# Performance work log

Measured on AMD Instinct MI355X. Metric: run time of the kernel, lower is better.

The kernel has to match this reference:

```python
import jax, jax.numpy as jnp
import numpy as np

B, T, C, H = 4, 4096, 1024, 64

def setup_inputs() -> dict:
    key = jax.random.key(0)
    k1, k2, k3, k4, k5 = jax.random.split(key, 5)
    scale = 0.02
    return {
        "x": jax.random.normal(k1, (B, T, C), dtype=jnp.float32),
        "head_bias": jax.random.normal(k2, (T, T), dtype=jnp.float32) * 0.1,
        "w_k": jax.random.normal(k3, (C, H), dtype=jnp.float32) * scale,
        "w_q": jax.random.normal(k4, (C, H), dtype=jnp.float32) * scale,
        "w_v": jax.random.normal(k5, (C, H), dtype=jnp.float32) * scale,
    }

def reference(x, head_bias, w_k, w_q, w_v):
    # x: (B,T,C) ; projections: (B,T,H)
    k = jnp.einsum('btc,ch->bth', x, w_k)
    q = jnp.einsum('btc,ch->bth', x, w_q)
    v = jnp.einsum('btc,ch->bth', x, w_v)
    Tq = x.shape[1]
    # scores: (B,T,T) with RPE bias and causal mask
    scores = jnp.einsum('bqh,bkh->bqk', q, k) * (k.shape[-1] ** -0.5)
    scores = scores + head_bias[None, :, :]
    causal = jnp.tril(jnp.ones((Tq, Tq), dtype=bool))
    scores = jnp.where(causal[None, :, :], scores, -jnp.inf)
    weights = jax.nn.softmax(scores, axis=-1)
    out = jnp.einsum('bqk,bkh->bqh', weights, v)
    return out
```

## Files before the change

kernel.cpp:

```cpp
#include <hip/hip_runtime.h>
#include <hip/hip_bf16.h>


#define T_DIM 4096
#define C_DIM 1024
#define QT    64
#define KT    64
#define CK    512

typedef __attribute__((ext_vector_type(8))) short s16x8;
typedef __attribute__((ext_vector_type(4))) float f32x4;
typedef __attribute__((ext_vector_type(2))) unsigned int u32x2;

__device__ __forceinline__ short f2bf(float f) {
    unsigned u = __builtin_bit_cast(unsigned, f);
    u += 0x7FFFu + ((u >> 16) & 1u);
    return (short)(u >> 16);
}
__device__ __forceinline__ unsigned pack2(float a, float b) {
    unsigned ua = __builtin_bit_cast(unsigned, a);
    unsigned ub = __builtin_bit_cast(unsigned, b);
    ua += 0x7FFFu + ((ua >> 16) & 1u);
    ub += 0x7FFFu + ((ub >> 16) & 1u);
    return __builtin_amdgcn_perm(ub, ua, 0x07060302u);
}
__device__ __forceinline__ float bf2f(short s) {
    unsigned u = ((unsigned)(unsigned short)s) << 16;
    return __builtin_bit_cast(float, u);
}

__global__ __launch_bounds__(256) void prep_frag(
    const float* __restrict__ wk, const float* __restrict__ wq,
    const float* __restrict__ wv, short* __restrict__ wfrag)
{
    int ksAll = blockIdx.x, mat = blockIdx.y;
    const float* w = (mat == 0) ? wk : ((mat == 1) ? wq : wv);
    float sc = (mat == 1) ? 0.125f : 1.0f;
    int nt = threadIdx.x >> 6, lane = threadIdx.x & 63;
    int quad = lane >> 4, l15 = lane & 15;
    int h = nt * 16 + l15;
    int cb = ksAll * 32 + quad * 8;
    s16x8 v;
    #pragma unroll
    for (int j = 0; j < 8; ++j) v[j] = f2bf(w[(cb + j) * 64 + h] * sc);
    *(s16x8*)&wfrag[((ksAll * 12 + mat * 4 + nt) * 64 + lane) * 8] = v;
}

__global__ __launch_bounds__(256, 2) void proj_part(
    const float* __restrict__ x, const short* __restrict__ wfrag,
    short* __restrict__ pp)
{
    int w = threadIdx.x >> 6, lane = threadIdx.x & 63;
    int l15 = lane & 15, quad = lane >> 4;
    int row0 = (blockIdx.x * 4 + w) * 16;
    int cq = blockIdx.y;

    f32x4 acc[12];
    #pragma unroll
    for (int i = 0; i < 12; ++i) acc[i] = (f32x4){0.f, 0.f, 0.f, 0.f};

    const float* xrow = x + (size_t)(row0 + l15) * C_DIM + cq * 256;

    #pragma unroll
    for (int ks = 0; ks < 8; ++ks) {
        int ksAll = cq * 8 + ks;
        const s16x8* fb = (const s16x8*)&wfrag[(size_t)(ksAll * 12 * 64 + lane) * 8];
        f32x4 x0 = *(const f32x4*)(xrow + ks * 32 + quad * 8);
        f32x4 x1 = *(const f32x4*)(xrow + ks * 32 + quad * 8 + 4);
        s16x8 af;
        unsigned p0 = pack2(x0[0], x0[1]), p1 = pack2(x0[2], x0[3]);
        unsigned p2 = pack2(x1[0], x1[1]), p3 = pack2(x1[2], x1[3]);
        af[0] = (short)p0; af[1] = (short)(p0 >> 16);
        af[2] = (short)p1; af[3] = (short)(p1 >> 16);
        af[4] = (short)p2; af[5] = (short)(p2 >> 16);
        af[6] = (short)p3; af[7] = (short)(p3 >> 16);
        #pragma unroll
        for (int f = 0; f < 12; ++f) {
            s16x8 bf = fb[f * 64];
            acc[f] = __builtin_amdgcn_mfma_f32_16x16x32_bf16(af, bf, acc[f], 0, 0, 0);
        }
    }
    short* base = pp + (size_t)cq * 16384 * 192;
    #pragma unroll
    for (int f = 0; f < 12; ++f) {
        int mat = f >> 2, nt = f & 3;
        #pragma unroll
        for (int r = 0; r < 4; ++r)
            base[(size_t)(row0 + quad * 4 + r) * 192 + mat * 64 + nt * 16 + l15] =
                f2bf(acc[f][r]);
    }
}

__global__ __launch_bounds__(256) void proj_combine(
    const short* __restrict__ pp, short* __restrict__ kb,
    short* __restrict__ qb, short* __restrict__ vtb)
{
    int m0 = blockIdx.x * 64;
    __shared__ short vt[64][72];
    #pragma unroll
    for (int o = 0; o < 6; ++o) {
        int oct = o * 256 + threadIdx.x;
        int row = oct / 24, c8 = (oct - row * 24) * 8;
        float s[8];
        #pragma unroll
        for (int j = 0; j < 8; ++j) s[j] = 0.f;
        #pragma unroll
        for (int cq = 0; cq < 4; ++cq) {
            s16x8 v = *(const s16x8*)&pp[((size_t)cq * 16384 + m0 + row) * 192 + c8];
            #pragma unroll
            for (int j = 0; j < 8; ++j) s[j] += bf2f(v[j]);
        }
        s16x8 r;
        #pragma unroll
        for (int j = 0; j < 4; ++j) {
            unsigned d = pack2(s[2 * j], s[2 * j + 1]);
            r[2 * j] = (short)d; r[2 * j + 1] = (short)(d >> 16);
        }
        if (c8 < 64)        *(s16x8*)&kb[(size_t)(m0 + row) * 64 + c8] = r;
        else if (c8 < 128)  *(s16x8*)&qb[(size_t)(m0 + row) * 64 + (c8 - 64)] = r;
        else {
            #pragma unroll
            for (int j = 0; j < 8; ++j) vt[c8 - 128 + j][row] = r[j];
        }
    }
    __syncthreads();
    int b = m0 >> 12, t0 = m0 & 4095;
    #pragma unroll
    for (int o = 0; o < 2; ++o) {
        int oct = o * 256 + threadIdx.x;
        int h = oct >> 3, tl = (oct & 7) * 8;
        s16x8 v = *(const s16x8*)&vt[h][tl];
        *(s16x8*)&vtb[(((size_t)b * 64 + h) << 12) + t0 + tl] = v;
    }
}

__global__ __launch_bounds__(256) void flash_part(
    const short* __restrict__ qb, const short* __restrict__ kb,
    const short* __restrict__ vtb, const float* __restrict__ bias,
    short* __restrict__ po)
{
    int qt = blockIdx.x, c = blockIdx.y, b = blockIdx.z;
    int q0 = qt * QT;
    int kstart = c * CK;
    int kend = min(kstart + CK, q0 + QT);
    if (kstart >= kend) return;

    __shared__ __align__(16) short klds[64][72];
    __shared__ __align__(16) short vlds[64][72];
    __shared__ __align__(16) short plds[4][16][72];

    int w = threadIdx.x >> 6, lane = threadIdx.x & 63;
    int l15 = lane & 15, quad = lane >> 4;
    int strip0 = q0 + w * 16;

    const short* qrow = qb + (size_t)(b * T_DIM + strip0 + l15) * 64;
    s16x8 aq0 = *(const s16x8*)(qrow + quad * 8);
    s16x8 aq1 = *(const s16x8*)(qrow + 32 + quad * 8);

    float l_sum = 0.f;
    f32x4 accO[4];
    #pragma unroll
    for (int nt = 0; nt < 4; ++nt) accO[nt] = (f32x4){0.f, 0.f, 0.f, 0.f};

    const float* brow = bias + (size_t)(strip0 + l15) * T_DIM;

    for (int k0 = kstart; k0 < kend; k0 += KT) {
        f32x4 vb[4];
        #pragma unroll
        for (int nt = 0; nt < 4; ++nt)
            vb[nt] = *(const f32x4*)&brow[k0 + nt * 16 + quad * 4];

        __syncthreads();
        #pragma unroll
        for (int rep = 0; rep < 4; ++rep) {
            int cid = threadIdx.x + rep * 256;
            int rem = cid & 511, row = rem >> 3, ch = rem & 7;
            if (cid < 512)
                *(s16x8*)&klds[row][ch * 8] =
                    *(const s16x8*)&kb[(size_t)(b * T_DIM + k0 + row) * 64 + ch * 8];
            else
                *(s16x8*)&vlds[row][ch * 8] =
                    *(const s16x8*)&vtb[(((size_t)b * 64 + row) << 12) + k0 + ch * 8];
        }
        __syncthreads();

        f32x4 accS[4];
        #pragma unroll
        for (int nt = 0; nt < 4; ++nt) accS[nt] = (f32x4){0.f, 0.f, 0.f, 0.f};
        #pragma unroll
        for (int nt = 0; nt < 4; ++nt) {
            s16x8 a0 = *(const s16x8*)&klds[nt * 16 + l15][quad * 8];
            accS[nt] = __builtin_amdgcn_mfma_f32_16x16x32_bf16(a0, aq0, accS[nt], 0, 0, 0);
            s16x8 a1 = *(const s16x8*)&klds[nt * 16 + l15][32 + quad * 8];
            accS[nt] = __builtin_amdgcn_mfma_f32_16x16x32_bf16(a1, aq1, accS[nt], 0, 0, 0);
        }

        int qrow_g = strip0 + l15;
        bool diag = (k0 + KT - 1 > strip0);
        #pragma unroll
        for (int nt = 0; nt < 4; ++nt) {
            float sv[4];
            #pragma unroll
            for (int r = 0; r < 4; ++r) {
                sv[r] = accS[nt][r] + vb[nt][r];
                if (diag && (k0 + nt * 16 + quad * 4 + r > qrow_g))
                    sv[r] = -__builtin_inff();
                float p = __expf(sv[r]);
                sv[r] = p;
                l_sum += p;
            }
            u32x2 d;
            d[0] = pack2(sv[0], sv[1]);
            d[1] = pack2(sv[2], sv[3]);
            *(u32x2*)&plds[w][l15][nt * 16 + quad * 4] = d;
        }

        s16x8 ap0 = *(const s16x8*)&plds[w][l15][quad * 8];
        s16x8 ap1 = *(const s16x8*)&plds[w][l15][32 + quad * 8];
        #pragma unroll
        for (int nt = 0; nt < 4; ++nt) {
            s16x8 bv0 = *(const s16x8*)&vlds[nt * 16 + l15][quad * 8];
            accO[nt] = __builtin_amdgcn_mfma_f32_16x16x32_bf16(ap0, bv0, accO[nt], 0, 0, 0);
            s16x8 bv1 = *(const s16x8*)&vlds[nt * 16 + l15][32 + quad * 8];
            accO[nt] = __builtin_amdgcn_mfma_f32_16x16x32_bf16(ap1, bv1, accO[nt], 0, 0, 0);
        }
    }

    l_sum += __shfl_xor(l_sum, 16, 64);
    l_sum += __shfl_xor(l_sum, 32, 64);

    short* base = po + (size_t)(((b * 64 + qt) * 8) + c) * 4160;
    #pragma unroll
    for (int nt = 0; nt < 4; ++nt)
        #pragma unroll
        for (int r = 0; r < 4; ++r)
            base[(w * 16 + quad * 4 + r) * 64 + nt * 16 + l15] = f2bf(accO[nt][r]);
    if (quad == 0) base[4096 + w * 16 + l15] = f2bf(l_sum);
}

__global__ __launch_bounds__(256) void flash_reduce(
    const short* __restrict__ po, float* __restrict__ out)
{
    int idx = blockIdx.x * 256 + threadIdx.x;
    int row = idx >> 4, c4 = idx & 15;
    int b = row >> 12, t = row & 4095;
    int qt = t >> 6, rloc = t & 63;
    int nc = (t >> 9) + 1;
    float o0 = 0.f, o1 = 0.f, o2 = 0.f, o3 = 0.f, l = 0.f;
    for (int cc = 0; cc < nc; ++cc) {
        const short* base = po + (size_t)(((b * 64 + qt) * 8) + cc) * 4160;
        const short* p = &base[rloc * 64 + c4 * 4];
        o0 += bf2f(p[0]); o1 += bf2f(p[1]); o2 += bf2f(p[2]); o3 += bf2f(p[3]);
        l += bf2f(base[4096 + rloc]);
    }
    float inv = 1.0f / l;
    f32x4 res = (f32x4){o0 * inv, o1 * inv, o2 * inv, o3 * inv};
    *(f32x4*)&out[(size_t)row * 64 + c4 * 4] = res;
}

extern "C" void kernel_launch(void* const* d_in, const int* in_sizes, int n_in,
                              void* d_out, int out_size, void* d_ws, size_t ws_size,
                              hipStream_t stream) {
    (void)in_sizes; (void)n_in; (void)out_size; (void)ws_size;
    const float* x    = (const float*)d_in[0];
    const float* bias = (const float*)d_in[1];
    const float* wk   = (const float*)d_in[2];
    const float* wq   = (const float*)d_in[3];
    const float* wv   = (const float*)d_in[4];
    float* out = (float*)d_out;

    short* wfrag = (short*)d_ws;
    short* kb    = wfrag + 196608;
    short* qb    = kb + 1048576;
    short* vtb   = qb + 1048576;
    short* pp    = vtb + 1048576;
    short* po    = pp + (size_t)12582912;

    prep_frag<<<dim3(32, 3), dim3(256), 0, stream>>>(wk, wq, wv, wfrag);
    proj_part<<<dim3(256, 4), dim3(256), 0, stream>>>(x, wfrag, pp);
    proj_combine<<<dim3(256), dim3(256), 0, stream>>>(pp, kb, qb, vtb);
    flash_part<<<dim3(64, 8, 4), dim3(256), 0, stream>>>(qb, kb, vtb, bias, po);
    flash_reduce<<<dim3(1024), dim3(256), 0, stream>>>(po, out);
}
```

Measured before the change: 221.8 us.

## Load K/V MFMA fragments directly from global memory, drop LDS staging

The flash kernel no longer stages K and V^T tiles through shared memory with two block barriers per tile. Each wave now loads its MFMA operand fragments straight from global memory, so the four waves fetch the same K/V data redundantly and rely on L1/L2 caching. The projection kernel drops its occupancy hint, stops unrolling the C-chunk loop, and rotates the starting chunk per block to spread weight-fragment reads. The trade is fewer barriers and less LDS traffic against more global/cache loads and higher register pressure.

```diff
diff --git a/kernel.cpp b/kernel.cpp
--- a/kernel.cpp
+++ b/kernel.cpp
@@ -46,7 +46,7 @@
     *(s16x8*)&wfrag[((ksAll * 12 + mat * 4 + nt) * 64 + lane) * 8] = v;
 }
 
-__global__ __launch_bounds__(256, 2) void proj_part(
+__global__ __launch_bounds__(256) void proj_part(
     const float* __restrict__ x, const short* __restrict__ wfrag,
     short* __restrict__ pp)
 {
@@ -61,8 +61,9 @@
 
     const float* xrow = x + (size_t)(row0 + l15) * C_DIM + cq * 256;
 
-    #pragma unroll
-    for (int ks = 0; ks < 8; ++ks) {
+    #pragma unroll 1
+    for (int ksi = 0; ksi < 8; ++ksi) {
+        int ks = (ksi + blockIdx.x) & 7;
         int ksAll = cq * 8 + ks;
         const s16x8* fb = (const s16x8*)&wfrag[(size_t)(ksAll * 12 * 64 + lane) * 8];
         f32x4 x0 = *(const f32x4*)(xrow + ks * 32 + quad * 8);
@@ -145,8 +146,6 @@
     int kend = min(kstart + CK, q0 + QT);
     if (kstart >= kend) return;
 
-    __shared__ __align__(16) short klds[64][72];
-    __shared__ __align__(16) short vlds[64][72];
     __shared__ __align__(16) short plds[4][16][72];
 
     int w = threadIdx.x >> 6, lane = threadIdx.x & 63;
@@ -163,36 +162,36 @@
     for (int nt = 0; nt < 4; ++nt) accO[nt] = (f32x4){0.f, 0.f, 0.f, 0.f};
 
     const float* brow = bias + (size_t)(strip0 + l15) * T_DIM;
-
+    const short* kbb  = kb + ((size_t)b * T_DIM) * 64;
+    const short* vbb  = vtb + ((size_t)b * 64 << 12);
+
+    #pragma unroll 1
     for (int k0 = kstart; k0 < kend; k0 += KT) {
+        s16x8 ak0[4], ak1[4];
+        #pragma unroll
+        for (int nt = 0; nt < 4; ++nt) {
+            const short* kr = kbb + (size_t)(k0 + nt * 16 + l15) * 64;
+            ak0[nt] = *(const s16x8*)(kr + quad * 8);
+            ak1[nt] = *(const s16x8*)(kr + 32 + quad * 8);
+        }
         f32x4 vb[4];
         #pragma unroll
         for (int nt = 0; nt < 4; ++nt)
             vb[nt] = *(const f32x4*)&brow[k0 + nt * 16 + quad * 4];
-
-        __syncthreads();
-        #pragma unroll
-        for (int rep = 0; rep < 4; ++rep) {
-            int cid = threadIdx.x + rep * 256;
-            int rem = cid & 511, row = rem >> 3, ch = rem & 7;
-            if (cid < 512)
-                *(s16x8*)&klds[row][ch * 8] =
-                    *(const s16x8*)&kb[(size_t)(b * T_DIM + k0 + row) * 64 + ch * 8];
-            else
-                *(s16x8*)&vlds[row][ch * 8] =
-                    *(const s16x8*)&vtb[(((size_t)b * 64 + row) << 12) + k0 + ch * 8];
-        }
-        __syncthreads();
+        s16x8 bv0[4], bv1[4];
+        #pragma unroll
+        for (int nt = 0; nt < 4; ++nt) {
+            const short* vr = vbb + ((size_t)(nt * 16 + l15) << 12) + k0;
+            bv0[nt] = *(const s16x8*)(vr + quad * 8);
+            bv1[nt] = *(const s16x8*)(vr + 32 + quad * 8);
+        }
 
         f32x4 accS[4];
         #pragma unroll
-        for (int nt = 0; nt < 4; ++nt) accS[nt] = (f32x4){0.f, 0.f, 0.f, 0.f};
-        #pragma unroll
-        for (int nt = 0; nt < 4; ++nt) {
-            s16x8 a0 = *(const s16x8*)&klds[nt * 16 + l15][quad * 8];
-            accS[nt] = __builtin_amdgcn_mfma_f32_16x16x32_bf16(a0, aq0, accS[nt], 0, 0, 0);
-            s16x8 a1 = *(const s16x8*)&klds[nt * 16 + l15][32 + quad * 8];
-            accS[nt] = __builtin_amdgcn_mfma_f32_16x16x32_bf16(a1, aq1, accS[nt], 0, 0, 0);
+        for (int nt = 0; nt < 4; ++nt) {
+            accS[nt] = (f32x4){0.f, 0.f, 0.f, 0.f};
+            accS[nt] = __builtin_amdgcn_mfma_f32_16x16x32_bf16(ak0[nt], aq0, accS[nt], 0, 0, 0);
+            accS[nt] = __builtin_amdgcn_mfma_f32_16x16x32_bf16(ak1[nt], aq1, accS[nt], 0, 0, 0);
         }
 
         int qrow_g = strip0 + l15;
@@ -219,10 +218,8 @@
         s16x8 ap1 = *(const s16x8*)&plds[w][l15][32 + quad * 8];
         #pragma unroll
         for (int nt = 0; nt < 4; ++nt) {
-            s16x8 bv0 = *(const s16x8*)&vlds[nt * 16 + l15][quad * 8];
-            accO[nt] = __builtin_amdgcn_mfma_f32_16x16x32_bf16(ap0, bv0, accO[nt], 0, 0, 0);
-            s16x8 bv1 = *(const s16x8*)&vlds[nt * 16 + l15][32 + quad * 8];
-            accO[nt] = __builtin_amdgcn_mfma_f32_16x16x32_bf16(ap1, bv1, accO[nt], 0, 0, 0);
+            accO[nt] = __builtin_amdgcn_mfma_f32_16x16x32_bf16(ap0, bv0[nt], accO[nt], 0, 0, 0);
+            accO[nt] = __builtin_amdgcn_mfma_f32_16x16x32_bf16(ap1, bv1[nt], accO[nt], 0, 0, 0);
         }
     }
 
```

New measurement: 306.5 us. +38.2%, slower.
